# Performance work log

Hardware: AMD Instinct MI355X
Metric: run time of the kernel (lower is better)

Reference implementation:

```python
import jax, jax.numpy as jnp
import numpy as np

B, T, C_FEAT, H = 1024, 256, 512, 256


def setup_inputs() -> dict:
    key = jax.random.key(0)
    ks = jax.random.split(key, 8)
    s_ih = 1.0 / np.sqrt(H)
    return {
        "features": jax.random.normal(ks[0], (B, T, C_FEAT), dtype=jnp.float32),
        "last_coord": jax.random.normal(ks[1], (B, 2), dtype=jnp.float32),
        "W_ih": jax.random.uniform(ks[2], (3 * H, C_FEAT + 2), jnp.float32, -s_ih, s_ih),
        "W_hh": jax.random.uniform(ks[3], (3 * H, H), jnp.float32, -s_ih, s_ih),
        "b_ih": jax.random.uniform(ks[4], (3 * H,), jnp.float32, -s_ih, s_ih),
        "b_hh": jax.random.uniform(ks[5], (3 * H,), jnp.float32, -s_ih, s_ih),
        "W_proj": jax.random.uniform(ks[6], (2, H), jnp.float32, -s_ih, s_ih),
        "b_proj": jax.random.uniform(ks[7], (2,), jnp.float32, -s_ih, s_ih),
    }


def reference(features, last_coord, W_ih, W_hh, b_ih, b_hh, W_proj, b_proj):
    # features: (B, T, C_feat); last_coord: (B, 2)
    Bb, Tt, Cf = features.shape
    Hh = W_hh.shape[1]
    h0 = jnp.zeros((Bb, Hh), dtype=features.dtype)

    def step(carry, feat_t):
        h, coord = carry
        x = jnp.concatenate([feat_t, coord], axis=1)          # (B, C+2)
        gi = x @ W_ih.T + b_ih                                 # (B, 3H)
        gh = h @ W_hh.T + b_hh                                 # (B, 3H)
        i_r, i_z, i_n = jnp.split(gi, 3, axis=1)
        h_r, h_z, h_n = jnp.split(gh, 3, axis=1)
        r = jax.nn.sigmoid(i_r + h_r)
        z = jax.nn.sigmoid(i_z + h_z)
        n = jnp.tanh(i_n + r * h_n)
        h_new = (1.0 - z) * n + z * h                          # PyTorch GRU update
        disp = h_new @ W_proj.T + b_proj                       # (B, 2)
        return (h_new, coord + disp), disp

    feats_t = jnp.swapaxes(features, 0, 1)                     # (T, B, C)
    _, disps = jax.lax.scan(step, (h0, last_coord), feats_t)   # (T, B, 2)
    return jnp.swapaxes(disps, 0, 1)                           # (B, T, 2)
```

## Files before the change

kernel.cpp:

```cpp
#include <hip/hip_runtime.h>
#include <stdint.h>

typedef unsigned short u16;
typedef unsigned int   u32;
typedef __attribute__((ext_vector_type(8))) __bf16 bf16x8;
typedef __attribute__((ext_vector_type(4))) float  f32x4;
typedef __attribute__((ext_vector_type(8))) u16    u16x8;
typedef __attribute__((ext_vector_type(4))) u16    u16x4;
typedef __attribute__((ext_vector_type(2))) u32    u32x2;

__device__ __forceinline__ u16 f2bf(float f) {
    u32 u = __float_as_uint(f);
    u32 r = (u + 0x7fffu + ((u >> 16) & 1u)) >> 16;
    return (u16)r;
}
__device__ __forceinline__ float bf2f(u16 v) { return __uint_as_float(((u32)v) << 16); }
__device__ __forceinline__ bf16x8 as_bf(u16x8 x) { union { u16x8 a; bf16x8 b; } u; u.a = x; return u.b; }
__device__ __forceinline__ void gload_lds16(const void* g, void* l) {
    __builtin_amdgcn_global_load_lds((const __attribute__((address_space(1))) void*)g,
                                     (__attribute__((address_space(3))) void*)l, 16, 0, 0);
}

__global__ void k_prep(const float* __restrict__ W_ih, const float* __restrict__ W_hh,
                       const float* __restrict__ b_ih, const float* __restrict__ b_hh,
                       u16* __restrict__ Wf, u16* __restrict__ Whh, float* __restrict__ bsum) {
    int i = blockIdx.x * 256 + threadIdx.x;
    if (i < 768 * 512) { int o = i >> 9, k = i & 511; Wf[i] = f2bf(W_ih[o * 514 + k]); }
    if (i < 768 * 256) { Whh[i] = f2bf(W_hh[i]); }
    if (i < 768)       { bsum[i] = b_ih[i] + (i < 512 ? b_hh[i] : 0.f); }
}

__global__ void k_cast(const float* __restrict__ f, u16* __restrict__ o) {
    const size_t N8 = (size_t)262144 * 512 / 8;
    for (size_t i = (size_t)blockIdx.x * 256 + threadIdx.x; i < N8; i += (size_t)gridDim.x * 256) {
        float4 a = ((const float4*)f)[i * 2];
        float4 b = ((const float4*)f)[i * 2 + 1];
        u16x8 v;
        v[0] = f2bf(a.x); v[1] = f2bf(a.y); v[2] = f2bf(a.z); v[3] = f2bf(a.w);
        v[4] = f2bf(b.x); v[5] = f2bf(b.y); v[6] = f2bf(b.z); v[7] = f2bf(b.w);
        ((u16x8*)o)[i] = v;
    }
}

__global__ __launch_bounds__(256) void k_gemm(const u16* __restrict__ featbf,
                                              const u16* __restrict__ Wf,
                                              const float* __restrict__ bsum,
                                              float* __restrict__ Gf) {
    __shared__ u16 As[128 * 64];
    __shared__ u16 Bs[128 * 64];
    const int tid = threadIdx.x;
    const int l = tid & 63, wv = tid >> 6;
    const int wr = wv >> 1, wc = wv & 1;
    const int lb = l & 15, lq = l >> 4;
    const int n0 = blockIdx.x * 128;
    const int m0 = blockIdx.y * 128;
    const int rl = l >> 3;
    const int c16 = (l & 7) * 16;
    const int sswz = (rl & 7) << 4;

    f32x4 acc[4][4] = {};

    for (int k0 = 0; k0 < 512; k0 += 64) {
        __syncthreads();
#pragma unroll
        for (int i = 0; i < 4; ++i) {
            int ci = wv * 4 + i;
            int r = ci * 8 + rl;
            const char* sa = (const char*)(featbf + (size_t)(m0 + r) * 512) + k0 * 2 + (c16 ^ sswz);
            gload_lds16(sa, (char*)As + ci * 1024);
            const char* sb = (const char*)(Wf + (size_t)(n0 + r) * 512) + k0 * 2 + (c16 ^ sswz);
            gload_lds16(sb, (char*)Bs + ci * 1024);
        }
        __syncthreads();
#pragma unroll
        for (int kc = 0; kc < 2; ++kc) {
            bf16x8 af[4], bfr[4];
#pragma unroll
            for (int mi = 0; mi < 4; ++mi) {
                int row = wr * 64 + mi * 16 + lb;
                af[mi] = *(const bf16x8*)((char*)As + row * 128 + (((kc * 32 + lq * 8) * 2) ^ ((row & 7) << 4)));
            }
#pragma unroll
            for (int ni = 0; ni < 4; ++ni) {
                int row = wc * 64 + ni * 16 + lb;
                bfr[ni] = *(const bf16x8*)((char*)Bs + row * 128 + (((kc * 32 + lq * 8) * 2) ^ ((row & 7) << 4)));
            }
#pragma unroll
            for (int mi = 0; mi < 4; ++mi)
#pragma unroll
                for (int ni = 0; ni < 4; ++ni)
                    acc[mi][ni] = __builtin_amdgcn_mfma_f32_16x16x32_bf16(af[mi], bfr[ni], acc[mi][ni], 0, 0, 0);
        }
    }
#pragma unroll
    for (int ni = 0; ni < 4; ++ni) {
        int o = n0 + wc * 64 + ni * 16 + lb;
        float bi = bsum[o];
#pragma unroll
        for (int mi = 0; mi < 4; ++mi) {
#pragma unroll
            for (int j = 0; j < 4; ++j) {
                int m = m0 + wr * 64 + mi * 16 + lq * 4 + j;
                int bb = m >> 8, tt = m & 255;
                Gf[(size_t)((tt << 10) + bb) * 768 + o] = acc[mi][ni][j] + bi;
            }
        }
    }
}

template<typename ST>
__global__ __launch_bounds__(256) void k_gemm_legacy(const float* __restrict__ feat,
                                                     const u16* __restrict__ Wf,
                                                     const float* __restrict__ bsum,
                                                     ST* __restrict__ Gf) {
    __shared__ u16 As[128 * 64];
    __shared__ u16 Bs[128 * 64];
    const int tid = threadIdx.x;
    const int l = tid & 63, wv = tid >> 6;
    const int wr = wv >> 1, wc = wv & 1;
    const int lb = l & 15, lq = l >> 4;
    const int n0 = blockIdx.x * 128;
    const int m0 = blockIdx.y * 128;
    const int srow = tid >> 1, scol = (tid & 1) * 32;

    f32x4 acc[4][4] = {};

    for (int k0 = 0; k0 < 512; k0 += 64) {
        __syncthreads();
        const float* ga = feat + (size_t)(m0 + srow) * 512 + k0 + scol;
        const u16*   gb = Wf + (n0 + srow) * 512 + k0 + scol;
        char* arow = (char*)As + srow * 128;
        char* brow = (char*)Bs + srow * 128;
        const int swz = (srow & 7) << 4;
#pragma unroll
        for (int i = 0; i < 4; ++i) {
            float4 f0 = *(const float4*)(ga + i * 8);
            float4 f1 = *(const float4*)(ga + i * 8 + 4);
            u16x8 v;
            v[0] = f2bf(f0.x); v[1] = f2bf(f0.y); v[2] = f2bf(f0.z); v[3] = f2bf(f0.w);
            v[4] = f2bf(f1.x); v[5] = f2bf(f1.y); v[6] = f2bf(f1.z); v[7] = f2bf(f1.w);
            *(u16x8*)(arow + (((scol + i * 8) * 2) ^ swz)) = v;
            u16x8 w8 = *(const u16x8*)(gb + i * 8);
            *(u16x8*)(brow + (((scol + i * 8) * 2) ^ swz)) = w8;
        }
        __syncthreads();
#pragma unroll
        for (int kc = 0; kc < 2; ++kc) {
            bf16x8 af[4], bfr[4];
#pragma unroll
            for (int mi = 0; mi < 4; ++mi) {
                int row = wr * 64 + mi * 16 + lb;
                af[mi] = *(const bf16x8*)((char*)As + row * 128 + (((kc * 32 + lq * 8) * 2) ^ ((row & 7) << 4)));
            }
#pragma unroll
            for (int ni = 0; ni < 4; ++ni) {
                int row = wc * 64 + ni * 16 + lb;
                bfr[ni] = *(const bf16x8*)((char*)Bs + row * 128 + (((kc * 32 + lq * 8) * 2) ^ ((row & 7) << 4)));
            }
#pragma unroll
            for (int mi = 0; mi < 4; ++mi)
#pragma unroll
                for (int ni = 0; ni < 4; ++ni)
                    acc[mi][ni] = __builtin_amdgcn_mfma_f32_16x16x32_bf16(af[mi], bfr[ni], acc[mi][ni], 0, 0, 0);
        }
    }
#pragma unroll
    for (int ni = 0; ni < 4; ++ni) {
        int o = n0 + wc * 64 + ni * 16 + lb;
        float bi = bsum[o];
#pragma unroll
        for (int mi = 0; mi < 4; ++mi) {
#pragma unroll
            for (int j = 0; j < 4; ++j) {
                int m = m0 + wr * 64 + mi * 16 + lq * 4 + j;
                int bb = m >> 8, tt = m & 255;
                size_t idx = (size_t)((tt << 10) + bb) * 768 + o;
                float v = acc[mi][ni][j] + bi;
                if constexpr (sizeof(ST) == 4) Gf[idx] = v; else Gf[idx] = f2bf(v);
            }
        }
    }
}

template<typename ST>
__global__ __launch_bounds__(512, 2) void k_rnn(const float* __restrict__ lastc,
                                                const float* __restrict__ W_ih,
                                                const float* __restrict__ bhh_g,
                                                const float* __restrict__ Wp,
                                                const float* __restrict__ bp,
                                                const u16* __restrict__ Whh,
                                                const ST* __restrict__ Gf,
                                                float* __restrict__ out) {
    __shared__ u16 Wlds[3 * 768 * 32];
    __shared__ u16 hbf[16 * 320];
    __shared__ float wpL[256 * 2];
    __shared__ float coordL[16 * 2];
    __shared__ float dPart[8 * 16 * 2];

    const int tid = threadIdx.x, l = tid & 63, wv = tid >> 6;
    const int lb = l & 15, lq = l >> 4;
    const int bb = blockIdx.x << 4;
    const int swz = (lb & 7) << 4;

    bf16x8 wres[5][3][2];
    bf16x8 wcf[3][2];
    float bhhn[2][4];
#pragma unroll
    for (int g = 0; g < 3; ++g)
#pragma unroll
        for (int ut = 0; ut < 2; ++ut) {
            int row = g * 256 + (2 * wv + ut) * 16 + lb;
#pragma unroll
            for (int kc = 0; kc < 5; ++kc)
                wres[kc][g][ut] = *(const bf16x8*)(Whh + row * 256 + kc * 32 + lq * 8);
            u16x8 cf = {0, 0, 0, 0, 0, 0, 0, 0};
            if (lq == 0) {
                cf[0] = f2bf(W_ih[row * 514 + 512]);
                cf[1] = f2bf(W_ih[row * 514 + 513]);
            }
            wcf[g][ut] = as_bf(cf);
        }
#pragma unroll
    for (int ut = 0; ut < 2; ++ut)
#pragma unroll
        for (int j = 0; j < 4; ++j)
            bhhn[ut][j] = bhh_g[512 + (2 * wv + ut) * 16 + lq * 4 + j];

    for (int i = tid; i < 3 * 768 * 16; i += 512) {
        int kcs = i / (768 * 16), rem = i - kcs * (768 * 16);
        int row = rem >> 4, kh = rem & 15;
        ((u32*)Wlds)[i] = *(const u32*)(Whh + row * 256 + (5 + kcs) * 32 + kh * 2);
    }
    for (int i = tid; i < 16 * 320 / 2; i += 512) ((u32*)hbf)[i] = 0u;
    if (tid < 256) { wpL[tid * 2] = Wp[tid]; wpL[tid * 2 + 1] = Wp[256 + tid]; }
    float bpc = (tid < 32) ? bp[tid & 1] : 0.f;
    __syncthreads();
    if (tid < 32) {
        int b = tid >> 1, c = tid & 1;
        float cc = lastc[(bb + b) * 2 + c];
        coordL[b * 2 + c] = cc;
        *(u16*)((char*)hbf + b * 640 + 512 + ((c * 2) ^ ((b & 7) << 4))) = f2bf(cc);
    }
    __syncthreads();

    float hreg[2][4] = {};
    const ST* gr = Gf + (size_t)(bb + lb) * 768 + lq * 4;
    const char* hrow = (const char*)hbf + lb * 640;

    for (int t = 0; t < 256; ++t) {
        float gf[3][2][4];
#pragma unroll
        for (int g = 0; g < 3; ++g)
#pragma unroll
            for (int ut = 0; ut < 2; ++ut) {
                int off = g * 256 + (2 * wv + ut) * 16;
                if constexpr (sizeof(ST) == 4) {
                    float4 v = *(const float4*)(gr + off);
                    gf[g][ut][0] = v.x; gf[g][ut][1] = v.y; gf[g][ut][2] = v.z; gf[g][ut][3] = v.w;
                } else {
                    u16x4 v = *(const u16x4*)(gr + off);
#pragma unroll
                    for (int j = 0; j < 4; ++j) gf[g][ut][j] = bf2f(v[j]);
                }
            }

        f32x4 acc[3][2] = {};
        f32x4 accC[2] = {};
#pragma unroll
        for (int kc = 0; kc < 5; ++kc) {
            bf16x8 hb = *(const bf16x8*)(hrow + ((kc * 64 + lq * 16) ^ swz));
#pragma unroll
            for (int g = 0; g < 3; ++g)
#pragma unroll
                for (int ut = 0; ut < 2; ++ut)
                    acc[g][ut] = __builtin_amdgcn_mfma_f32_16x16x32_bf16(wres[kc][g][ut], hb, acc[g][ut], 0, 0, 0);
        }
#pragma unroll
        for (int kcs = 0; kcs < 3; ++kcs) {
            bf16x8 hb = *(const bf16x8*)(hrow + (((5 + kcs) * 64 + lq * 16) ^ swz));
#pragma unroll
            for (int g = 0; g < 3; ++g)
#pragma unroll
                for (int ut = 0; ut < 2; ++ut) {
                    int row = g * 256 + (2 * wv + ut) * 16 + lb;
                    bf16x8 wl = *(const bf16x8*)((const char*)Wlds + (size_t)(kcs * 768 + row) * 64 + lq * 16);
                    acc[g][ut] = __builtin_amdgcn_mfma_f32_16x16x32_bf16(wl, hb, acc[g][ut], 0, 0, 0);
                }
        }
        {
            bf16x8 hbE = *(const bf16x8*)(hrow + 512 + ((lq * 16) ^ swz));
#pragma unroll
            for (int ut = 0; ut < 2; ++ut) {
                acc[0][ut] = __builtin_amdgcn_mfma_f32_16x16x32_bf16(wcf[0][ut], hbE, acc[0][ut], 0, 0, 0);
                acc[1][ut] = __builtin_amdgcn_mfma_f32_16x16x32_bf16(wcf[1][ut], hbE, acc[1][ut], 0, 0, 0);
                accC[ut]   = __builtin_amdgcn_mfma_f32_16x16x32_bf16(wcf[2][ut], hbE, accC[ut],   0, 0, 0);
            }
        }
        __syncthreads();

        float pd0 = 0.f, pd1 = 0.f;
#pragma unroll
        for (int ut = 0; ut < 2; ++ut) {
            int ub = (2 * wv + ut) * 16 + lq * 4;
            float4 wpa = *(const float4*)(wpL + ub * 2);
            float4 wpb = *(const float4*)(wpL + ub * 2 + 4);
            u16 hpk[4];
#pragma unroll
            for (int j = 0; j < 4; ++j) {
                float r = 1.f / (1.f + __expf(-(gf[0][ut][j] + acc[0][ut][j])));
                float z = 1.f / (1.f + __expf(-(gf[1][ut][j] + acc[1][ut][j])));
                float ghn = acc[2][ut][j] + bhhn[ut][j];
                float xn = gf[2][ut][j] + accC[ut][j] + r * ghn;
                float e = __expf(-2.f * fabsf(xn));
                float th = (1.f - e) / (1.f + e);
                th = (xn >= 0.f) ? th : -th;
                float hn = (1.f - z) * th + z * hreg[ut][j];
                hreg[ut][j] = hn;
                float w0 = (j == 0) ? wpa.x : (j == 1) ? wpa.z : (j == 2) ? wpb.x : wpb.z;
                float w1 = (j == 0) ? wpa.y : (j == 1) ? wpa.w : (j == 2) ? wpb.y : wpb.w;
                pd0 += w0 * hn;
                pd1 += w1 * hn;
                hpk[j] = f2bf(hn);
            }
            u32x2 pv;
            pv.x = (u32)hpk[0] | ((u32)hpk[1] << 16);
            pv.y = (u32)hpk[2] | ((u32)hpk[3] << 16);
            *(u32x2*)((char*)hbf + lb * 640 + ((ub * 2) ^ swz)) = pv;
        }
        pd0 += __shfl_xor(pd0, 16); pd0 += __shfl_xor(pd0, 32);
        pd1 += __shfl_xor(pd1, 16); pd1 += __shfl_xor(pd1, 32);
        if (l < 16) { dPart[(wv * 16 + l) * 2] = pd0; dPart[(wv * 16 + l) * 2 + 1] = pd1; }
        __syncthreads();

        if (tid < 32) {
            int b = tid >> 1, c = tid & 1;
            float d = bpc;
#pragma unroll
            for (int w8 = 0; w8 < 8; ++w8) d += dPart[(w8 * 16 + b) * 2 + c];
            out[((size_t)(bb + b) * 256 + t) * 2 + c] = d;
            float nc = coordL[b * 2 + c] + d;
            coordL[b * 2 + c] = nc;
            *(u16*)((char*)hbf + b * 640 + 512 + ((c * 2) ^ ((b & 7) << 4))) = f2bf(nc);
        }
        __syncthreads();
        gr += (size_t)1024 * 768;
    }
}

extern "C" void kernel_launch(void* const* d_in, const int* in_sizes, int n_in,
                              void* d_out, int out_size, void* d_ws, size_t ws_size,
                              hipStream_t stream) {
    const float* feat   = (const float*)d_in[0];
    const float* lastc  = (const float*)d_in[1];
    const float* W_ih   = (const float*)d_in[2];
    const float* W_hh   = (const float*)d_in[3];
    const float* b_ih   = (const float*)d_in[4];
    const float* b_hh   = (const float*)d_in[5];
    const float* W_proj = (const float*)d_in[6];
    const float* b_proj = (const float*)d_in[7];
    float* out = (float*)d_out;

    char* ws = (char*)d_ws;
    u16*   Wf    = (u16*)ws;
    u16*   Whh   = (u16*)(ws + 786432);
    float* bsum  = (float*)(ws + 786432 + 393216);
    const size_t off_fb = 786432 + 393216 + 3072;
    u16*   featbf = (u16*)(ws + off_fb);
    const size_t off_gf_full = off_fb + (size_t)262144 * 512 * 2;
    const size_t need_full  = off_gf_full + (size_t)262144 * 768 * 4;
    const size_t need_tier2 = off_fb + (size_t)262144 * 768 * 4;
    const size_t need_tier3 = off_fb + (size_t)262144 * 768 * 2;

    k_prep<<<1536, 256, 0, stream>>>(W_ih, W_hh, b_ih, b_hh, Wf, Whh, bsum);

    if (ws_size >= need_full) {
        float* Gf = (float*)(ws + off_gf_full);
        k_cast<<<16384, 256, 0, stream>>>(feat, featbf);
        k_gemm<<<dim3(6, 2048), 256, 0, stream>>>(featbf, Wf, bsum, Gf);
        k_rnn<float><<<64, 512, 0, stream>>>(lastc, W_ih, b_hh, W_proj, b_proj, Whh, Gf, out);
    } else if (ws_size >= need_tier2) {
        float* Gf = (float*)(ws + off_fb);
        k_gemm_legacy<float><<<dim3(6, 2048), 256, 0, stream>>>(feat, Wf, bsum, Gf);
        k_rnn<float><<<64, 512, 0, stream>>>(lastc, W_ih, b_hh, W_proj, b_proj, Whh, Gf, out);
    } else {
        u16* Gf = (u16*)(ws + off_fb);
        (void)need_tier3;
        k_gemm_legacy<u16><<<dim3(6, 2048), 256, 0, stream>>>(feat, Wf, bsum, Gf);
        k_rnn<u16><<<64, 512, 0, stream>>>(lastc, W_ih, b_hh, W_proj, b_proj, Whh, Gf, out);
    }
}
```

Measured before the change: 1.482 ms.

## Remap GEMM blocks across XCDs, relayout RNN LDS weights, defer output stores

Adds an XCD-aware block index remap to the input-projection GEMMs so consecutive logical tiles land on the same chiplet, aiming to improve L2 reuse of the shared weight tiles. Reorganizes the LDS copy of the recurrent weight slice so each wave reads one contiguous 1 KB fragment per MFMA operand, which removes strided row-indexed LDS reads and likely bank conflicts. Also moves each step's displacement store to the start of the next step, keeping the global write off the critical path before the barrier. The remap assumes the grid size divides evenly across eight XCDs.

```diff
diff --git a/kernel.cpp b/kernel.cpp
--- a/kernel.cpp
+++ b/kernel.cpp
@@ -8,6 +8,7 @@
 typedef __attribute__((ext_vector_type(8))) u16    u16x8;
 typedef __attribute__((ext_vector_type(4))) u16    u16x4;
 typedef __attribute__((ext_vector_type(2))) u32    u32x2;
+typedef __attribute__((ext_vector_type(2))) float  f32x2;
 
 __device__ __forceinline__ u16 f2bf(float f) {
     u32 u = __float_as_uint(f);
@@ -40,6 +41,13 @@
         v[4] = f2bf(b.x); v[5] = f2bf(b.y); v[6] = f2bf(b.z); v[7] = f2bf(b.w);
         ((u16x8*)o)[i] = v;
     }
+}
+
+__device__ __forceinline__ void xcd_remap(int& n0, int& m0) {
+    int phys = blockIdx.x + blockIdx.y * 6;
+    int logical = (phys & 7) * 1536 + (phys >> 3);
+    n0 = (logical % 6) * 128;
+    m0 = (logical / 6) * 128;
 }
 
 __global__ __launch_bounds__(256) void k_gemm(const u16* __restrict__ featbf,
@@ -52,8 +60,7 @@
     const int l = tid & 63, wv = tid >> 6;
     const int wr = wv >> 1, wc = wv & 1;
     const int lb = l & 15, lq = l >> 4;
-    const int n0 = blockIdx.x * 128;
-    const int m0 = blockIdx.y * 128;
+    int n0, m0; xcd_remap(n0, m0);
     const int rl = l >> 3;
     const int c16 = (l & 7) * 16;
     const int sswz = (rl & 7) << 4;
@@ -119,8 +126,7 @@
     const int l = tid & 63, wv = tid >> 6;
     const int wr = wv >> 1, wc = wv & 1;
     const int lb = l & 15, lq = l >> 4;
-    const int n0 = blockIdx.x * 128;
-    const int m0 = blockIdx.y * 128;
+    int n0, m0; xcd_remap(n0, m0);
     const int srow = tid >> 1, scol = (tid & 1) * 32;
 
     f32x4 acc[4][4] = {};
@@ -191,7 +197,7 @@
                                                 const u16* __restrict__ Whh,
                                                 const ST* __restrict__ Gf,
                                                 float* __restrict__ out) {
-    __shared__ u16 Wlds[3 * 768 * 32];
+    __shared__ u16 Wlds[144 * 512];
     __shared__ u16 hbf[16 * 320];
     __shared__ float wpL[256 * 2];
     __shared__ float coordL[16 * 2];
@@ -226,10 +232,12 @@
         for (int j = 0; j < 4; ++j)
             bhhn[ut][j] = bhh_g[512 + (2 * wv + ut) * 16 + lq * 4 + j];
 
-    for (int i = tid; i < 3 * 768 * 16; i += 512) {
-        int kcs = i / (768 * 16), rem = i - kcs * (768 * 16);
-        int row = rem >> 4, kh = rem & 15;
-        ((u32*)Wlds)[i] = *(const u32*)(Whh + row * 256 + (5 + kcs) * 32 + kh * 2);
+    for (int i = tid; i < 36864; i += 512) {
+        int s = i >> 8, r = i & 255, ll = r >> 2, e2 = r & 3;
+        int g = s / 48, rem = s - g * 48, tt = rem / 3, kcs = rem - tt * 3;
+        int row = g * 256 + tt * 16 + (ll & 15);
+        int k = (5 + kcs) * 32 + (ll >> 4) * 8 + e2 * 2;
+        ((u32*)Wlds)[i] = *(const u32*)(Whh + row * 256 + k);
     }
     for (int i = tid; i < 16 * 320 / 2; i += 512) ((u32*)hbf)[i] = 0u;
     if (tid < 256) { wpL[tid * 2] = Wp[tid]; wpL[tid * 2 + 1] = Wp[256 + tid]; }
@@ -244,10 +252,14 @@
     __syncthreads();
 
     float hreg[2][4] = {};
+    float prevD = 0.f;
     const ST* gr = Gf + (size_t)(bb + lb) * 768 + lq * 4;
     const char* hrow = (const char*)hbf + lb * 640;
 
     for (int t = 0; t < 256; ++t) {
+        if (t > 0 && tid < 32)
+            out[((size_t)(bb + (tid >> 1)) * 256 + (t - 1)) * 2 + (tid & 1)] = prevD;
+
         float gf[3][2][4];
 #pragma unroll
         for (int g = 0; g < 3; ++g)
@@ -282,8 +294,8 @@
             for (int g = 0; g < 3; ++g)
 #pragma unroll
                 for (int ut = 0; ut < 2; ++ut) {
-                    int row = g * 256 + (2 * wv + ut) * 16 + lb;
-                    bf16x8 wl = *(const bf16x8*)((const char*)Wlds + (size_t)(kcs * 768 + row) * 64 + lq * 16);
+                    int s = (g * 16 + 2 * wv + ut) * 3 + kcs;
+                    bf16x8 wl = *(const bf16x8*)((const char*)Wlds + s * 1024 + l * 16);
                     acc[g][ut] = __builtin_amdgcn_mfma_f32_16x16x32_bf16(wl, hb, acc[g][ut], 0, 0, 0);
                 }
         }
@@ -337,7 +349,7 @@
             float d = bpc;
 #pragma unroll
             for (int w8 = 0; w8 < 8; ++w8) d += dPart[(w8 * 16 + b) * 2 + c];
-            out[((size_t)(bb + b) * 256 + t) * 2 + c] = d;
+            prevD = d;
             float nc = coordL[b * 2 + c] + d;
             coordL[b * 2 + c] = nc;
             *(u16*)((char*)hbf + b * 640 + 512 + ((c * 2) ^ ((b & 7) << 4))) = f2bf(nc);
@@ -345,6 +357,8 @@
         __syncthreads();
         gr += (size_t)1024 * 768;
     }
+    if (tid < 32)
+        out[((size_t)(bb + (tid >> 1)) * 256 + 255) * 2 + (tid & 1)] = prevD;
 }
 
 extern "C" void kernel_launch(void* const* d_in, const int* in_sizes, int n_in,
@@ -369,7 +383,6 @@
     const size_t off_gf_full = off_fb + (size_t)262144 * 512 * 2;
     const size_t need_full  = off_gf_full + (size_t)262144 * 768 * 4;
     const size_t need_tier2 = off_fb + (size_t)262144 * 768 * 4;
-    const size_t need_tier3 = off_fb + (size_t)262144 * 768 * 2;
 
     k_prep<<<1536, 256, 0, stream>>>(W_ih, W_hh, b_ih, b_hh, Wf, Whh, bsum);
 
@@ -384,7 +397,6 @@
         k_rnn<float><<<64, 512, 0, stream>>>(lastc, W_ih, b_hh, W_proj, b_proj, Whh, Gf, out);
     } else {
         u16* Gf = (u16*)(ws + off_fb);
-        (void)need_tier3;
         k_gemm_legacy<u16><<<dim3(6, 2048), 256, 0, stream>>>(feat, Wf, bsum, Gf);
         k_rnn<u16><<<64, 512, 0, stream>>>(lastc, W_ih, b_hh, W_proj, b_proj, Whh, Gf, out);
     }
```

New measurement: 1.511 ms. No clear change (+1.9%).
